# Kernel tuning notes

Hardware: AMD Instinct MI355X
Metric: run time of the kernel (lower is better)

The kernel has to match this reference:

```python
import jax, jax.numpy as jnp
import numpy as np

D_CONV = 4
DT_RANK = 64
D_STATE = 16


def setup_inputs() -> dict:
    key = jax.random.key(0)
    ks = jax.random.split(key, 10)
    d_model, d_in, L, B = 1024, 2048, 1024, 2
    s = 0.02
    x = jax.random.normal(ks[0], (B, L, d_model), jnp.float32)
    W_in = jax.random.normal(ks[1], (d_model, 2 * d_in), jnp.float32) * s
    conv_w = jax.random.normal(ks[2], (D_CONV, 1, d_in), jnp.float32) * s
    conv_b = jax.random.normal(ks[3], (d_in,), jnp.float32) * s
    W_x = jax.random.normal(ks[4], (d_in, DT_RANK + 2 * D_STATE), jnp.float32) * s
    W_dt = jax.random.normal(ks[5], (DT_RANK, d_in), jnp.float32) * s
    b_dt = jax.random.normal(ks[6], (d_in,), jnp.float32) * s
    A_log = jnp.log(jnp.tile(jnp.arange(1, D_STATE + 1, dtype=jnp.float32), (d_in, 1)))
    D = jnp.ones((d_in,), jnp.float32)
    W_out = jax.random.normal(ks[7], (d_in, d_model), jnp.float32) * s
    return {"x": x, "W_in": W_in, "conv_w": conv_w, "conv_b": conv_b,
            "W_x": W_x, "W_dt": W_dt, "b_dt": b_dt, "A_log": A_log, "D": D,
            "W_out": W_out}


def _selective_scan(u, delta, A, Bm, Cm, D):
    # u, delta: [b,l,d]; A: [d,n]; Bm, Cm: [b,l,n]; D: [d]
    b, l, d = u.shape
    n = A.shape[1]
    deltaA = jnp.exp(jnp.einsum('bld,dn->bldn', delta, A))          # [b,l,d,n]
    dBu = delta[..., None] * Bm[:, :, None, :] * u[..., None]        # [b,l,d,n]

    def step(state, inp):
        dA_t, dBu_t, C_t = inp                                       # [b,d,n],[b,d,n],[b,n]
        state = dA_t * state + dBu_t
        y_t = jnp.einsum('bdn,bn->bd', state, C_t)
        return state, y_t

    init = jnp.zeros((b, d, n), u.dtype)
    xs = (jnp.swapaxes(deltaA, 0, 1), jnp.swapaxes(dBu, 0, 1), jnp.swapaxes(Cm, 0, 1))
    _, ys = jax.lax.scan(step, init, xs)                             # [l,b,d]
    y = jnp.swapaxes(ys, 0, 1)
    return y + u * D


def reference(x, W_in, conv_w, conv_b, W_x, W_dt, b_dt, A_log, D, W_out):
    B, L, _ = x.shape
    d_in = W_in.shape[1] // 2

    x_and_res = x @ W_in                                             # [B,L,2*d_in]
    x_, res = jnp.split(x_and_res, [d_in], axis=-1)

    # depthwise causal conv over the projected branch
    x_pad = jnp.pad(x_, ((0, 0), (D_CONV - 1, 0), (0, 0)))
    x_conv = jax.lax.conv_general_dilated(
        x_pad, conv_w, window_strides=(1,), padding='VALID',
        dimension_numbers=('NWC', 'WIO', 'NWC'), feature_group_count=d_in)
    x_conv = x_conv[:, :L, :] + conv_b
    x_conv = jax.nn.silu(x_conv)

    # ssm
    A = -jnp.exp(A_log)                                              # [d_in,n]
    x_dbl = x_conv @ W_x                                             # [B,L,dt_rank+2n]
    delta, Bm, Cm = jnp.split(x_dbl, [DT_RANK, DT_RANK + D_STATE], axis=-1)
    delta = jax.nn.softplus(delta @ W_dt + b_dt)                     # [B,L,d_in]
    y = _selective_scan(x_conv, delta, A, Bm, Cm, D)

    y = y * jax.nn.silu(res)
    return y @ W_out
```

## Files before the change

kernel.cpp:

```cpp
#include <hip/hip_runtime.h>
#include <hip/hip_bf16.h>
#include <math.h>


typedef unsigned short u16;
typedef short s16;
typedef float f32x4 __attribute__((ext_vector_type(4)));
typedef s16 bf16x8 __attribute__((ext_vector_type(8)));

#define LDS_CAST(p) ((__attribute__((address_space(3))) void*)(p))
#define GLB_CAST(p) ((const __attribute__((address_space(1))) void*)(p))

#define LL 1024
#define DI 2048
#define NC 64
#define LC 16

#define OFF_FLAG   0u
#define OFF_CX     256u
#define OFF_CCW    4194560u
#define OFF_CCB    4211200u
#define OFF_CBDT   4215296u
#define OFF_CALOG  4219392u
#define OFF_CD     4284928u
#define OFF_WINT   4289024u
#define OFF_WOUTT  12677632u
#define OFF_WXT    16871936u
#define OFF_WDTT   17265152u
#define OFF_XRP    17527296u
#define OFF_P      (OFF_XRP + 0u)
#define OFF_YBF    (OFF_XRP + 0u)
#define OFF_S      (OFF_XRP + 16777216u)
#define OFF_SIN    (OFF_XRP + 33554432u)
#define OFF_YP     (OFF_XRP + 16777216u)
#define OFF_RESACT 84636160u
#define OFF_XCB    101413376u
#define OFF_XDBLP  109801984u
#define OFF_XDBL   116093440u
#define OFF_DELTA  116486656u

static __device__ __forceinline__ float b2f(u16 h) {
  return __uint_as_float(((unsigned)h) << 16);
}
static __device__ __forceinline__ u16 f2b(float f) {
  unsigned u = __float_as_uint(f);
  u += 0x7fffu + ((u >> 16) & 1u);
  return (u16)(u >> 16);
}

__global__ __launch_bounds__(256) void detect_dtype(
    const u16* __restrict__ x, const void* __restrict__ alog, int* flag) {
  __shared__ int cnt;
  if (threadIdx.x == 0) cnt = 0;
  __syncthreads();
  int good = 0;
#pragma unroll
  for (int j = 0; j < 16; j++) {
    u16 v = x[threadIdx.x * 16 + j];
    int e = (v >> 7) & 0xFF;
    good += (e >= 100 && e <= 140) ? 1 : 0;
  }
  atomicAdd(&cnt, good);
  __syncthreads();
  if (threadIdx.x == 0) {
    int fp32in = (cnt < 3600) ? 1 : 0;
    flag[0] = fp32in;
    int structured = fp32in;
    if (fp32in) {
      const float* af = (const float*)alog;
#pragma unroll
      for (int n = 0; n < 16; n++) {
        float a0 = __expf(af[n]);
        float a1 = __expf(af[777 * 16 + n]);
        float t = (float)(n + 1);
        if (fabsf(a0 - t) > 0.01f * t || fabsf(a1 - t) > 0.01f * t) structured = 0;
      }
    }
    flag[1] = structured;
  }
}

__global__ __launch_bounds__(256) void prep_inputs(
    const void* sx, const void* scw, const void* scb, const void* sbdt,
    const void* salog, const void* sd,
    const void* Win, const void* Wx, const void* Wdt, const void* Wout,
    char* __restrict__ ws, const int* __restrict__ flag) {
  const int fl = flag[0];
  int bid = blockIdx.x;
  if (bid < 8376) {
    long i = (long)bid * 256 + threadIdx.x;
    if (i >= 2144256) return;
    const void* src; u16* dst; long j;
    if (i < 2097152)      { src = sx;    dst = (u16*)(ws + OFF_CX);    j = i; }
    else if (i < 2105344) { src = scw;   dst = (u16*)(ws + OFF_CCW);   j = i - 2097152; }
    else if (i < 2107392) { src = scb;   dst = (u16*)(ws + OFF_CCB);   j = i - 2105344; }
    else if (i < 2109440) { src = sbdt;  dst = (u16*)(ws + OFF_CBDT);  j = i - 2107392; }
    else if (i < 2142208) { src = salog; dst = (u16*)(ws + OFF_CALOG); j = i - 2109440; }
    else                  { src = sd;    dst = (u16*)(ws + OFF_CD);    j = i - 2142208; }
    dst[j] = fl ? f2b(((const float*)src)[j]) : ((const u16*)src)[j];
    return;
  }
  bid -= 8376;
  const void* src; u16* dst; int R, C, tx_, ty_;
  if (bid < 4096)      { src=Win;  dst=(u16*)(ws+OFF_WINT);  R=1024; C=4096; ty_=bid/128; tx_=bid%128; }
  else if (bid < 6144) { bid-=4096; src=Wout; dst=(u16*)(ws+OFF_WOUTT); R=2048; C=1024; ty_=bid/32; tx_=bid%32; }
  else if (bid < 6336) { bid-=6144; src=Wx;   dst=(u16*)(ws+OFF_WXT);   R=2048; C=96;   ty_=bid/3;  tx_=bid%3; }
  else                 { bid-=6336; src=Wdt;  dst=(u16*)(ws+OFF_WDTT);  R=64;   C=2048; ty_=bid/64; tx_=bid%64; }
  __shared__ u16 tile[32][33];
  int tx = threadIdx.x & 31, ty = threadIdx.x >> 5;
  int c0 = tx_*32, r0 = ty_*32;
#pragma unroll
  for (int i = 0; i < 4; i++) {
    int r = r0 + ty + i*8, c = c0 + tx;
    if (r < R && c < C) {
      size_t off = (size_t)r*C + c;
      tile[ty + i*8][tx] = fl ? f2b(((const float*)src)[off]) : ((const u16*)src)[off];
    }
  }
  __syncthreads();
#pragma unroll
  for (int i = 0; i < 4; i++) {
    int c = c0 + ty + i*8, r = r0 + tx;
    if (r < R && c < C) dst[(size_t)c*R + r] = tile[tx][ty + i*8];
  }
}

__global__ __launch_bounds__(256) void gemm128split(
    const u16* __restrict__ A, const u16* __restrict__ Bt,
    float* __restrict__ Cout, int M, int N, int lda, int kslice) {
  __shared__ u16 sA[128*32];
  __shared__ u16 sB[128*32];
  const int tid = threadIdx.x;
  const int lane = tid & 63, w = tid >> 6;
  const int ln = lane & 15, q = lane >> 4;
  const int wr = w >> 1, wc = w & 1;
  const int m0 = blockIdx.y * 128, n0 = blockIdx.x * 128;
  const int kstart = blockIdx.z * kslice, kend = kstart + kslice;
  Cout += (size_t)blockIdx.z * M * N;
  const int li0 = tid, li1 = tid + 256;
  const int r0s = li0 >> 2, k0s = (li0 & 3) * 8;
  const int r1s = li1 >> 2, k1s = (li1 & 3) * 8;
  f32x4 acc[4][4] = {};
  for (int k0 = kstart; k0 < kend; k0 += 32) {
    __syncthreads();
    __builtin_amdgcn_global_load_lds(GLB_CAST(A + (size_t)(m0 + r0s)*lda + k0 + k0s), LDS_CAST(&sA[(size_t)li0*8]), 16, 0, 0);
    __builtin_amdgcn_global_load_lds(GLB_CAST(A + (size_t)(m0 + r1s)*lda + k0 + k1s), LDS_CAST(&sA[(size_t)li1*8]), 16, 0, 0);
    __builtin_amdgcn_global_load_lds(GLB_CAST(Bt + (size_t)(n0 + r0s)*lda + k0 + k0s), LDS_CAST(&sB[(size_t)li0*8]), 16, 0, 0);
    __builtin_amdgcn_global_load_lds(GLB_CAST(Bt + (size_t)(n0 + r1s)*lda + k0 + k1s), LDS_CAST(&sB[(size_t)li1*8]), 16, 0, 0);
    __syncthreads();
    bf16x8 af[4], bfr[4];
#pragma unroll
    for (int i = 0; i < 4; i++) {
      af[i]  = *(const bf16x8*)&sA[(wr*64 + i*16 + ln)*32 + q*8];
      bfr[i] = *(const bf16x8*)&sB[(wc*64 + i*16 + ln)*32 + q*8];
    }
#pragma unroll
    for (int mi = 0; mi < 4; mi++)
#pragma unroll
      for (int ni = 0; ni < 4; ni++)
        acc[mi][ni] = __builtin_amdgcn_mfma_f32_16x16x32_bf16(af[mi], bfr[ni], acc[mi][ni], 0, 0, 0);
  }
#pragma unroll
  for (int mi = 0; mi < 4; mi++)
#pragma unroll
    for (int ni = 0; ni < 4; ni++)
#pragma unroll
      for (int r = 0; r < 4; r++) {
        int m = m0 + wr*64 + mi*16 + q*4 + r;
        int n = n0 + wc*64 + ni*16 + ln;
        Cout[(size_t)m*N + n] = acc[mi][ni][r];
      }
}

__global__ __launch_bounds__(256) void conv_silu_res(
    const float* __restrict__ xrP, const u16* __restrict__ cw, const u16* __restrict__ cb,
    u16* __restrict__ xcb, float* __restrict__ resact) {
  const float* xr0 = xrP;
  const float* xr1 = xrP + (size_t)2048*4096;
  int idx = blockIdx.x * 256 + threadIdx.x;
  if (idx < 4194304) {
    int d = idx & (DI - 1);
    int row = idx >> 11;
    int l = row & (LL - 1);
    float acc = b2f(cb[d]);
#pragma unroll
    for (int j = 0; j < 4; j++) {
      int ls = l - 3 + j;
      if (ls >= 0) {
        size_t o = (size_t)(row - 3 + j)*4096 + d;
        acc += b2f(cw[j*DI + d]) * (xr0[o] + xr1[o]);
      }
    }
    if (!(acc == acc)) acc = 0.f;
    float t = fminf(fmaxf(acc, -80.f), 80.f);
    float v = acc / (1.f + __expf(-t));
    xcb[idx] = f2b(v);
  } else {
    int j = idx - 4194304;
    int d = j & (DI - 1);
    int row = j >> 11;
    size_t o = (size_t)row*4096 + 2048 + d;
    float res = xr0[o] + xr1[o];
    if (!(res == res)) res = 0.f;
    float t = fminf(fmaxf(res, -80.f), 80.f);
    resact[j] = res / (1.f + __expf(-t));
  }
}

__global__ __launch_bounds__(256) void xdbl_split(
    const u16* __restrict__ A, const u16* __restrict__ Bt, float* __restrict__ outP) {
  int wg = blockIdx.x * 4 + (threadIdx.x >> 6);
  int lane = threadIdx.x & 63, ln = lane & 15, q = lane >> 4;
  int mt = wg / 48, rem = wg % 48;
  int nt = rem >> 3, ks = rem & 7;
  const u16* ap = A  + (size_t)(mt*16 + ln)*2048 + ks*256 + q*8;
  const u16* bp = Bt + (size_t)(nt*16 + ln)*2048 + ks*256 + q*8;
  f32x4 acc = {};
#pragma unroll
  for (int k0 = 0; k0 < 256; k0 += 32) {
    bf16x8 a = *(const bf16x8*)(ap + k0);
    bf16x8 b = *(const bf16x8*)(bp + k0);
    acc = __builtin_amdgcn_mfma_f32_16x16x32_bf16(a, b, acc, 0, 0, 0);
  }
#pragma unroll
  for (int r = 0; r < 4; r++)
    outP[((size_t)ks*2048 + mt*16 + q*4 + r)*96 + nt*16 + ln] = acc[r];
}

__global__ __launch_bounds__(256) void xdbl_reduce(
    const float* __restrict__ outP, u16* __restrict__ xdbl) {
  int i = blockIdx.x * 256 + threadIdx.x;
  float s = 0.f;
#pragma unroll
  for (int ks = 0; ks < 8; ks++) s += outP[(size_t)ks*196608 + i];
  xdbl[i] = f2b(s);
}

__global__ __launch_bounds__(256) void gemm_delta(
    const u16* __restrict__ xdbl, const u16* __restrict__ WdtT,
    const u16* __restrict__ bdt, float* __restrict__ delta) {
  int w = (blockIdx.x * 256 + threadIdx.x) >> 6;
  int lane = threadIdx.x & 63, ln = lane & 15, q = lane >> 4;
  int mt = w & 127, nt = w >> 7;
  const u16* ap = xdbl + (size_t)(mt*16 + ln)*96 + q*8;
  const u16* bp = WdtT + (size_t)(nt*16 + ln)*64 + q*8;
  f32x4 acc = {};
#pragma unroll
  for (int k0 = 0; k0 < 64; k0 += 32) {
    bf16x8 a = *(const bf16x8*)(ap + k0);
    bf16x8 b = *(const bf16x8*)(bp + k0);
    acc = __builtin_amdgcn_mfma_f32_16x16x32_bf16(a, b, acc, 0, 0, 0);
  }
#pragma unroll
  for (int r = 0; r < 4; r++) {
    int m = mt*16 + q*4 + r, n = nt*16 + ln;
    float v = acc[r] + b2f(bdt[n]);
    if (!(v == v)) v = 0.f;
    float sp = (v > 15.f) ? v : log1pf(__expf(fmaxf(v, -80.f)));
    delta[(size_t)m*DI + n] = sp;
  }
}

__global__ __launch_bounds__(256) void scan_p1(
    const float* __restrict__ delta, const u16* __restrict__ xcb,
    const u16* __restrict__ xdbl, const u16* __restrict__ Alog,
    float* __restrict__ P, float* __restrict__ S, const int* __restrict__ flag) {
  const int structured = flag[1];
  int bid = blockIdx.x;
  int b = bid >> 9, r = bid & 511;
  int chunk = r >> 3, dblk = r & 7;
  int d = dblk*256 + threadIdx.x;
  float s[16], p[16];
#pragma unroll
  for (int n = 0; n < 16; n++) { s[n] = 0.f; p[n] = 1.f; }
  int row0 = b*LL + chunk*LC;
  if (structured) {
    for (int l = 0; l < LC; l++) {
      int row = row0 + l;
      float dl = delta[(size_t)row*DI + d];
      float du = dl * b2f(xcb[(size_t)row*DI + d]);
      const u16* bq = xdbl + (size_t)row*96 + 64;
      bf16x8 bv0 = *(const bf16x8*)(bq);
      bf16x8 bv1 = *(const bf16x8*)(bq + 8);
      float e1 = __expf(-dl);
      float dAc = 1.f;
#pragma unroll
      for (int n = 0; n < 8; n++) {
        dAc *= e1;
        s[n] = dAc * s[n] + du * b2f((u16)bv0[n]);
        p[n] *= dAc;
      }
#pragma unroll
      for (int n = 0; n < 8; n++) {
        dAc *= e1;
        s[n+8] = dAc * s[n+8] + du * b2f((u16)bv1[n]);
        p[n+8] *= dAc;
      }
    }
  } else {
    float Av[16];
#pragma unroll
    for (int n = 0; n < 16; n++) Av[n] = -__expf(fminf(b2f(Alog[d*16 + n]), 80.f));
    for (int l = 0; l < LC; l++) {
      int row = row0 + l;
      float dl = delta[(size_t)row*DI + d];
      float du = dl * b2f(xcb[(size_t)row*DI + d]);
      const u16* bq = xdbl + (size_t)row*96 + 64;
      bf16x8 bv0 = *(const bf16x8*)(bq);
      bf16x8 bv1 = *(const bf16x8*)(bq + 8);
#pragma unroll
      for (int n = 0; n < 8; n++) {
        float dA = __expf(fmaxf(dl * Av[n], -80.f));
        s[n] = dA * s[n] + du * b2f((u16)bv0[n]);
        p[n] *= dA;
      }
#pragma unroll
      for (int n = 0; n < 8; n++) {
        float dA = __expf(fmaxf(dl * Av[n+8], -80.f));
        s[n+8] = dA * s[n+8] + du * b2f((u16)bv1[n]);
        p[n+8] *= dA;
      }
    }
  }
  size_t o = ((size_t)(b*NC + chunk)*DI + d) * 16;
#pragma unroll
  for (int n = 0; n < 16; n++) { P[o + n] = p[n]; S[o + n] = s[n]; }
}

__global__ __launch_bounds__(256) void scan_p2(
    const float* __restrict__ P, const float* __restrict__ S, float* __restrict__ sIn) {
  int idx = blockIdx.x * 256 + threadIdx.x;
  int n = idx & 15, d = (idx >> 4) & (DI - 1), b = idx >> 15;
  float s = 0.f;
  for (int c = 0; c < NC; c++) {
    size_t o = ((size_t)(b*NC + c)*DI + d)*16 + n;
    sIn[o] = s;
    s = P[o] * s + S[o];
  }
}

__global__ __launch_bounds__(256) void scan_p3(
    const float* __restrict__ delta, const u16* __restrict__ xcb,
    const u16* __restrict__ xdbl, const u16* __restrict__ Alog,
    const u16* __restrict__ Dp, const float* __restrict__ resact,
    const float* __restrict__ sIn, u16* __restrict__ ybf, const int* __restrict__ flag) {
  const int structured = flag[1];
  int bid = blockIdx.x;
  int b = bid >> 9, r = bid & 511;
  int chunk = r >> 3, dblk = r & 7;
  int d = dblk*256 + threadIdx.x;
  float Dv = b2f(Dp[d]);
  float s[16];
  size_t o = ((size_t)(b*NC + chunk)*DI + d) * 16;
#pragma unroll
  for (int n = 0; n < 16; n++) s[n] = sIn[o + n];
  int row0 = b*LL + chunk*LC;
  if (structured) {
    for (int l = 0; l < LC; l++) {
      int row = row0 + l;
      float dl = delta[(size_t)row*DI + d];
      float u  = b2f(xcb[(size_t)row*DI + d]);
      float du = dl * u;
      const u16* bq = xdbl + (size_t)row*96 + 64;
      bf16x8 bv0 = *(const bf16x8*)(bq);
      bf16x8 bv1 = *(const bf16x8*)(bq + 8);
      bf16x8 cv0 = *(const bf16x8*)(bq + 16);
      bf16x8 cv1 = *(const bf16x8*)(bq + 24);
      float e1 = __expf(-dl);
      float dAc = 1.f;
      float y = 0.f;
#pragma unroll
      for (int n = 0; n < 8; n++) {
        dAc *= e1;
        s[n] = dAc * s[n] + du * b2f((u16)bv0[n]);
        y += s[n] * b2f((u16)cv0[n]);
      }
#pragma unroll
      for (int n = 0; n < 8; n++) {
        dAc *= e1;
        s[n+8] = dAc * s[n+8] + du * b2f((u16)bv1[n]);
        y += s[n+8] * b2f((u16)cv1[n]);
      }
      y += u * Dv;
      float out = y * resact[(size_t)row*DI + d];
      if (!(out == out)) out = 0.f;
      ybf[(size_t)row*DI + d] = f2b(out);
    }
  } else {
    float Av[16];
#pragma unroll
    for (int n = 0; n < 16; n++) Av[n] = -__expf(fminf(b2f(Alog[d*16 + n]), 80.f));
    for (int l = 0; l < LC; l++) {
      int row = row0 + l;
      float dl = delta[(size_t)row*DI + d];
      float u  = b2f(xcb[(size_t)row*DI + d]);
      float du = dl * u;
      const u16* bq = xdbl + (size_t)row*96 + 64;
      bf16x8 bv0 = *(const bf16x8*)(bq);
      bf16x8 bv1 = *(const bf16x8*)(bq + 8);
      bf16x8 cv0 = *(const bf16x8*)(bq + 16);
      bf16x8 cv1 = *(const bf16x8*)(bq + 24);
      float y = 0.f;
#pragma unroll
      for (int n = 0; n < 8; n++) {
        float dA = __expf(fmaxf(dl * Av[n], -80.f));
        s[n] = dA * s[n] + du * b2f((u16)bv0[n]);
        y += s[n] * b2f((u16)cv0[n]);
      }
#pragma unroll
      for (int n = 0; n < 8; n++) {
        float dA = __expf(fmaxf(dl * Av[n+8], -80.f));
        s[n+8] = dA * s[n+8] + du * b2f((u16)bv1[n]);
        y += s[n+8] * b2f((u16)cv1[n]);
      }
      y += u * Dv;
      float out = y * resact[(size_t)row*DI + d];
      if (!(out == out)) out = 0.f;
      ybf[(size_t)row*DI + d] = f2b(out);
    }
  }
}

__global__ __launch_bounds__(256) void out_reduce(
    const float* __restrict__ yP, void* __restrict__ out, const int* __restrict__ flag) {
  const int fl = flag[0];
  int i = blockIdx.x * 256 + threadIdx.x;
  float v = 0.f;
#pragma unroll
  for (int z = 0; z < 4; z++) v += yP[(size_t)z*2097152 + i];
  if (!(v == v)) v = 0.f;
  if (fl) ((float*)out)[i] = v;
  else    ((u16*)out)[i] = f2b(v);
}

extern "C" void kernel_launch(void* const* d_in, const int* in_sizes, int n_in,
                              void* d_out, int out_size, void* d_ws, size_t ws_size,
                              hipStream_t stream) {
  char* ws = (char*)d_ws;
  int*   flag   = (int*)  (ws + OFF_FLAG);
  u16*   cx     = (u16*)  (ws + OFF_CX);
  u16*   ccw    = (u16*)  (ws + OFF_CCW);
  u16*   ccb    = (u16*)  (ws + OFF_CCB);
  u16*   cbdt   = (u16*)  (ws + OFF_CBDT);
  u16*   cAlog  = (u16*)  (ws + OFF_CALOG);
  u16*   cD     = (u16*)  (ws + OFF_CD);
  u16*   WinT   = (u16*)  (ws + OFF_WINT);
  u16*   WoutT  = (u16*)  (ws + OFF_WOUTT);
  u16*   WxT    = (u16*)  (ws + OFF_WXT);
  u16*   WdtT   = (u16*)  (ws + OFF_WDTT);
  float* xrP    = (float*)(ws + OFF_XRP);
  float* resact = (float*)(ws + OFF_RESACT);
  u16*   xcb    = (u16*)  (ws + OFF_XCB);
  float* xdblP  = (float*)(ws + OFF_XDBLP);
  u16*   xdbl   = (u16*)  (ws + OFF_XDBL);
  float* delta  = (float*)(ws + OFF_DELTA);
  u16*   ybf    = (u16*)  (ws + OFF_YBF);
  float* P      = (float*)(ws + OFF_P);
  float* S      = (float*)(ws + OFF_S);
  float* sIn    = (float*)(ws + OFF_SIN);
  float* yP     = (float*)(ws + OFF_YP);

  detect_dtype<<<1, 256, 0, stream>>>((const u16*)d_in[0], d_in[7], flag);
  prep_inputs<<<14840, 256, 0, stream>>>(
      d_in[0], d_in[2], d_in[3], d_in[6], d_in[7], d_in[8],
      d_in[1], d_in[4], d_in[5], d_in[9], ws, flag);
  gemm128split<<<dim3(32, 16, 2), 256, 0, stream>>>(cx, WinT, xrP, 2048, 4096, 1024, 512);
  conv_silu_res<<<32768, 256, 0, stream>>>(xrP, ccw, ccb, xcb, resact);
  xdbl_split<<<1536, 256, 0, stream>>>(xcb, WxT, xdblP);
  xdbl_reduce<<<768, 256, 0, stream>>>(xdblP, xdbl);
  gemm_delta<<<4096, 256, 0, stream>>>(xdbl, WdtT, cbdt, delta);
  scan_p1<<<1024, 256, 0, stream>>>(delta, xcb, xdbl, cAlog, P, S, flag);
  scan_p2<<<256, 256, 0, stream>>>(P, S, sIn);
  scan_p3<<<1024, 256, 0, stream>>>(delta, xcb, xdbl, cAlog, cD, resact, sIn, ybf, flag);
  gemm128split<<<dim3(8, 16, 4), 256, 0, stream>>>(ybf, WoutT, yP, 2048, 1024, 2048, 512);
  out_reduce<<<8192, 256, 0, stream>>>(yP, d_out, flag);
}
```

Before: 265.1 us.

## Store intermediates in bf16 and compress structured-A chunk decay to one scalar

Split-K GEMM partials, the residual activation, delta and the output partials are now stored as bf16 instead of fp32. This halves memory traffic through the elementwise, scan and reduce kernels. For the structured A case (A_n = -(n+1)), scan_p1 now writes a single per-channel chunk decay product, and scan_p2 rebuilds each state's decay as q^(n+1), which cuts the P traffic by sixteen. The cost is lower precision from rounding split-K partials and delta to bf16, and a log2/exp2 reconstruction of the decay.

```diff
diff --git a/kernel.cpp b/kernel.cpp
--- a/kernel.cpp
+++ b/kernel.cpp
@@ -19,25 +19,26 @@
 #define OFF_FLAG   0u
 #define OFF_CX     256u
 #define OFF_CCW    4194560u
-#define OFF_CCB    4211200u
-#define OFF_CBDT   4215296u
-#define OFF_CALOG  4219392u
-#define OFF_CD     4284928u
-#define OFF_WINT   4289024u
-#define OFF_WOUTT  12677632u
-#define OFF_WXT    16871936u
-#define OFF_WDTT   17265152u
-#define OFF_XRP    17527296u
-#define OFF_P      (OFF_XRP + 0u)
-#define OFF_YBF    (OFF_XRP + 0u)
-#define OFF_S      (OFF_XRP + 16777216u)
-#define OFF_SIN    (OFF_XRP + 33554432u)
-#define OFF_YP     (OFF_XRP + 16777216u)
-#define OFF_RESACT 84636160u
-#define OFF_XCB    101413376u
-#define OFF_XDBLP  109801984u
-#define OFF_XDBL   116093440u
-#define OFF_DELTA  116486656u
+#define OFF_CCB    4210944u
+#define OFF_CBDT   4215040u
+#define OFF_CALOG  4219136u
+#define OFF_CD     4284672u
+#define OFF_WINT   4288768u
+#define OFF_WOUTT  12677376u
+#define OFF_WXT    16871680u
+#define OFF_WDTT   17264896u
+#define OFF_XRP    17527040u
+#define OFF_XCB    51081472u
+#define OFF_RESACT 59470080u
+#define OFF_XDBLP  67858688u
+#define OFF_XDBL   74150144u
+#define OFF_DELTA  74543360u
+#define OFF_P      82931968u
+#define OFF_PQ     99709184u
+#define OFF_S      100757760u
+#define OFF_SIN    117534976u
+#define OFF_YBF    134312192u
+#define OFF_YP     142700800u
 
 static __device__ __forceinline__ float b2f(u16 h) {
   return __uint_as_float(((unsigned)h) << 16);
@@ -127,7 +128,7 @@
 
 __global__ __launch_bounds__(256) void gemm128split(
     const u16* __restrict__ A, const u16* __restrict__ Bt,
-    float* __restrict__ Cout, int M, int N, int lda, int kslice) {
+    u16* __restrict__ Cout, int M, int N, int lda, int kslice) {
   __shared__ u16 sA[128*32];
   __shared__ u16 sB[128*32];
   const int tid = threadIdx.x;
@@ -168,15 +169,15 @@
       for (int r = 0; r < 4; r++) {
         int m = m0 + wr*64 + mi*16 + q*4 + r;
         int n = n0 + wc*64 + ni*16 + ln;
-        Cout[(size_t)m*N + n] = acc[mi][ni][r];
+        Cout[(size_t)m*N + n] = f2b(acc[mi][ni][r]);
       }
 }
 
 __global__ __launch_bounds__(256) void conv_silu_res(
-    const float* __restrict__ xrP, const u16* __restrict__ cw, const u16* __restrict__ cb,
-    u16* __restrict__ xcb, float* __restrict__ resact) {
-  const float* xr0 = xrP;
-  const float* xr1 = xrP + (size_t)2048*4096;
+    const u16* __restrict__ xrP, const u16* __restrict__ cw, const u16* __restrict__ cb,
+    u16* __restrict__ xcb, u16* __restrict__ resact) {
+  const u16* xr0 = xrP;
+  const u16* xr1 = xrP + (size_t)2048*4096;
   int idx = blockIdx.x * 256 + threadIdx.x;
   if (idx < 4194304) {
     int d = idx & (DI - 1);
@@ -188,7 +189,7 @@
       int ls = l - 3 + j;
       if (ls >= 0) {
         size_t o = (size_t)(row - 3 + j)*4096 + d;
-        acc += b2f(cw[j*DI + d]) * (xr0[o] + xr1[o]);
+        acc += b2f(cw[j*DI + d]) * (b2f(xr0[o]) + b2f(xr1[o]));
       }
     }
     if (!(acc == acc)) acc = 0.f;
@@ -200,10 +201,10 @@
     int d = j & (DI - 1);
     int row = j >> 11;
     size_t o = (size_t)row*4096 + 2048 + d;
-    float res = xr0[o] + xr1[o];
+    float res = b2f(xr0[o]) + b2f(xr1[o]);
     if (!(res == res)) res = 0.f;
     float t = fminf(fmaxf(res, -80.f), 80.f);
-    resact[j] = res / (1.f + __expf(-t));
+    resact[j] = f2b(res / (1.f + __expf(-t)));
   }
 }
 
@@ -238,7 +239,7 @@
 
 __global__ __launch_bounds__(256) void gemm_delta(
     const u16* __restrict__ xdbl, const u16* __restrict__ WdtT,
-    const u16* __restrict__ bdt, float* __restrict__ delta) {
+    const u16* __restrict__ bdt, u16* __restrict__ delta) {
   int w = (blockIdx.x * 256 + threadIdx.x) >> 6;
   int lane = threadIdx.x & 63, ln = lane & 15, q = lane >> 4;
   int mt = w & 127, nt = w >> 7;
@@ -257,53 +258,56 @@
     float v = acc[r] + b2f(bdt[n]);
     if (!(v == v)) v = 0.f;
     float sp = (v > 15.f) ? v : log1pf(__expf(fmaxf(v, -80.f)));
-    delta[(size_t)m*DI + n] = sp;
+    delta[(size_t)m*DI + n] = f2b(sp);
   }
 }
 
 __global__ __launch_bounds__(256) void scan_p1(
-    const float* __restrict__ delta, const u16* __restrict__ xcb,
+    const u16* __restrict__ delta, const u16* __restrict__ xcb,
     const u16* __restrict__ xdbl, const u16* __restrict__ Alog,
-    float* __restrict__ P, float* __restrict__ S, const int* __restrict__ flag) {
+    float* __restrict__ P, float* __restrict__ Pq, float* __restrict__ S,
+    const int* __restrict__ flag) {
   const int structured = flag[1];
   int bid = blockIdx.x;
   int b = bid >> 9, r = bid & 511;
   int chunk = r >> 3, dblk = r & 7;
   int d = dblk*256 + threadIdx.x;
-  float s[16], p[16];
-#pragma unroll
-  for (int n = 0; n < 16; n++) { s[n] = 0.f; p[n] = 1.f; }
+  float s[16];
+#pragma unroll
+  for (int n = 0; n < 16; n++) s[n] = 0.f;
   int row0 = b*LL + chunk*LC;
+  size_t o = ((size_t)(b*NC + chunk)*DI + d) * 16;
   if (structured) {
+    float qacc = 1.f;
     for (int l = 0; l < LC; l++) {
       int row = row0 + l;
-      float dl = delta[(size_t)row*DI + d];
+      float dl = b2f(delta[(size_t)row*DI + d]);
       float du = dl * b2f(xcb[(size_t)row*DI + d]);
       const u16* bq = xdbl + (size_t)row*96 + 64;
       bf16x8 bv0 = *(const bf16x8*)(bq);
       bf16x8 bv1 = *(const bf16x8*)(bq + 8);
       float e1 = __expf(-dl);
+      qacc *= e1;
       float dAc = 1.f;
 #pragma unroll
       for (int n = 0; n < 8; n++) {
         dAc *= e1;
         s[n] = dAc * s[n] + du * b2f((u16)bv0[n]);
-        p[n] *= dAc;
       }
 #pragma unroll
       for (int n = 0; n < 8; n++) {
         dAc *= e1;
         s[n+8] = dAc * s[n+8] + du * b2f((u16)bv1[n]);
-        p[n+8] *= dAc;
-      }
-    }
+      }
+    }
+    Pq[(size_t)(b*NC + chunk)*DI + d] = qacc;
   } else {
-    float Av[16];
-#pragma unroll
-    for (int n = 0; n < 16; n++) Av[n] = -__expf(fminf(b2f(Alog[d*16 + n]), 80.f));
+    float Av[16], p[16];
+#pragma unroll
+    for (int n = 0; n < 16; n++) { Av[n] = -__expf(fminf(b2f(Alog[d*16 + n]), 80.f)); p[n] = 1.f; }
     for (int l = 0; l < LC; l++) {
       int row = row0 + l;
-      float dl = delta[(size_t)row*DI + d];
+      float dl = b2f(delta[(size_t)row*DI + d]);
       float du = dl * b2f(xcb[(size_t)row*DI + d]);
       const u16* bq = xdbl + (size_t)row*96 + 64;
       bf16x8 bv0 = *(const bf16x8*)(bq);
@@ -321,28 +325,39 @@
         p[n+8] *= dA;
       }
     }
-  }
-  size_t o = ((size_t)(b*NC + chunk)*DI + d) * 16;
-#pragma unroll
-  for (int n = 0; n < 16; n++) { P[o + n] = p[n]; S[o + n] = s[n]; }
+#pragma unroll
+    for (int n = 0; n < 16; n++) P[o + n] = p[n];
+  }
+#pragma unroll
+  for (int n = 0; n < 16; n++) S[o + n] = s[n];
 }
 
 __global__ __launch_bounds__(256) void scan_p2(
-    const float* __restrict__ P, const float* __restrict__ S, float* __restrict__ sIn) {
+    const float* __restrict__ P, const float* __restrict__ Pq,
+    const float* __restrict__ S, float* __restrict__ sIn, const int* __restrict__ flag) {
+  const int structured = flag[1];
   int idx = blockIdx.x * 256 + threadIdx.x;
   int n = idx & 15, d = (idx >> 4) & (DI - 1), b = idx >> 15;
   float s = 0.f;
+  float np1 = (float)(n + 1);
   for (int c = 0; c < NC; c++) {
     size_t o = ((size_t)(b*NC + c)*DI + d)*16 + n;
     sIn[o] = s;
-    s = P[o] * s + S[o];
+    float pv;
+    if (structured) {
+      float qv = Pq[(size_t)(b*NC + c)*DI + d];
+      pv = exp2f(np1 * log2f(qv));
+    } else {
+      pv = P[o];
+    }
+    s = pv * s + S[o];
   }
 }
 
 __global__ __launch_bounds__(256) void scan_p3(
-    const float* __restrict__ delta, const u16* __restrict__ xcb,
+    const u16* __restrict__ delta, const u16* __restrict__ xcb,
     const u16* __restrict__ xdbl, const u16* __restrict__ Alog,
-    const u16* __restrict__ Dp, const float* __restrict__ resact,
+    const u16* __restrict__ Dp, const u16* __restrict__ resact,
     const float* __restrict__ sIn, u16* __restrict__ ybf, const int* __restrict__ flag) {
   const int structured = flag[1];
   int bid = blockIdx.x;
@@ -358,7 +373,7 @@
   if (structured) {
     for (int l = 0; l < LC; l++) {
       int row = row0 + l;
-      float dl = delta[(size_t)row*DI + d];
+      float dl = b2f(delta[(size_t)row*DI + d]);
       float u  = b2f(xcb[(size_t)row*DI + d]);
       float du = dl * u;
       const u16* bq = xdbl + (size_t)row*96 + 64;
@@ -382,7 +397,7 @@
         y += s[n+8] * b2f((u16)cv1[n]);
       }
       y += u * Dv;
-      float out = y * resact[(size_t)row*DI + d];
+      float out = y * b2f(resact[(size_t)row*DI + d]);
       if (!(out == out)) out = 0.f;
       ybf[(size_t)row*DI + d] = f2b(out);
     }
@@ -392,7 +407,7 @@
     for (int n = 0; n < 16; n++) Av[n] = -__expf(fminf(b2f(Alog[d*16 + n]), 80.f));
     for (int l = 0; l < LC; l++) {
       int row = row0 + l;
-      float dl = delta[(size_t)row*DI + d];
+      float dl = b2f(delta[(size_t)row*DI + d]);
       float u  = b2f(xcb[(size_t)row*DI + d]);
       float du = dl * u;
       const u16* bq = xdbl + (size_t)row*96 + 64;
@@ -414,7 +429,7 @@
         y += s[n+8] * b2f((u16)cv1[n]);
       }
       y += u * Dv;
-      float out = y * resact[(size_t)row*DI + d];
+      float out = y * b2f(resact[(size_t)row*DI + d]);
       if (!(out == out)) out = 0.f;
       ybf[(size_t)row*DI + d] = f2b(out);
     }
@@ -422,12 +437,12 @@
 }
 
 __global__ __launch_bounds__(256) void out_reduce(
-    const float* __restrict__ yP, void* __restrict__ out, const int* __restrict__ flag) {
+    const u16* __restrict__ yP, void* __restrict__ out, const int* __restrict__ flag) {
   const int fl = flag[0];
   int i = blockIdx.x * 256 + threadIdx.x;
   float v = 0.f;
 #pragma unroll
-  for (int z = 0; z < 4; z++) v += yP[(size_t)z*2097152 + i];
+  for (int z = 0; z < 4; z++) v += b2f(yP[(size_t)z*2097152 + i]);
   if (!(v == v)) v = 0.f;
   if (fl) ((float*)out)[i] = v;
   else    ((u16*)out)[i] = f2b(v);
@@ -448,17 +463,18 @@
   u16*   WoutT  = (u16*)  (ws + OFF_WOUTT);
   u16*   WxT    = (u16*)  (ws + OFF_WXT);
   u16*   WdtT   = (u16*)  (ws + OFF_WDTT);
-  float* xrP    = (float*)(ws + OFF_XRP);
-  float* resact = (float*)(ws + OFF_RESACT);
+  u16*   xrP    = (u16*)  (ws + OFF_XRP);
+  u16*   resact = (u16*)  (ws + OFF_RESACT);
   u16*   xcb    = (u16*)  (ws + OFF_XCB);
   float* xdblP  = (float*)(ws + OFF_XDBLP);
   u16*   xdbl   = (u16*)  (ws + OFF_XDBL);
-  float* delta  = (float*)(ws + OFF_DELTA);
-  u16*   ybf    = (u16*)  (ws + OFF_YBF);
+  u16*   delta  = (u16*)  (ws + OFF_DELTA);
   float* P      = (float*)(ws + OFF_P);
+  float* Pq     = (float*)(ws + OFF_PQ);
   float* S      = (float*)(ws + OFF_S);
   float* sIn    = (float*)(ws + OFF_SIN);
-  float* yP     = (float*)(ws + OFF_YP);
+  u16*   ybf    = (u16*)  (ws + OFF_YBF);
+  u16*   yP     = (u16*)  (ws + OFF_YP);
 
   detect_dtype<<<1, 256, 0, stream>>>((const u16*)d_in[0], d_in[7], flag);
   prep_inputs<<<14840, 256, 0, stream>>>(
@@ -469,8 +485,8 @@
   xdbl_split<<<1536, 256, 0, stream>>>(xcb, WxT, xdblP);
   xdbl_reduce<<<768, 256, 0, stream>>>(xdblP, xdbl);
   gemm_delta<<<4096, 256, 0, stream>>>(xdbl, WdtT, cbdt, delta);
-  scan_p1<<<1024, 256, 0, stream>>>(delta, xcb, xdbl, cAlog, P, S, flag);
-  scan_p2<<<256, 256, 0, stream>>>(P, S, sIn);
+  scan_p1<<<1024, 256, 0, stream>>>(delta, xcb, xdbl, cAlog, P, Pq, S, flag);
+  scan_p2<<<256, 256, 0, stream>>>(P, Pq, S, sIn, flag);
   scan_p3<<<1024, 256, 0, stream>>>(delta, xcb, xdbl, cAlog, cD, resact, sIn, ybf, flag);
   gemm128split<<<dim3(8, 16, 4), 256, 0, stream>>>(ybf, WoutT, yP, 2048, 1024, 2048, 512);
   out_reduce<<<8192, 256, 0, stream>>>(yP, d_out, flag);
```

New measurement: 284.8 us. +7.4%, slower.
